# Optimization experiments

Hardware: AMD Instinct MI355X
Metric: run time of the kernel (lower is better)

Reference implementation:

```python
import jax, jax.numpy as jnp
import numpy as np

B, S, D, H, E = 4, 2048, 1024, 4096, 8


def setup_inputs() -> dict:
    key = jax.random.key(0)
    ks = jax.random.split(key, 8)
    w = lambda k, shape: (jax.random.normal(k, shape, jnp.float32) * 0.02)
    return {
        "x": jax.random.normal(ks[0], (B, S, D), jnp.float32),
        "noise_eps": jax.random.normal(ks[1], (B, S, E), jnp.float32),
        "Wg": w(ks[2], (D, E)), "bg": jnp.zeros((E,), jnp.float32),
        "Wn": w(ks[3], (D, E)), "bn": jnp.zeros((E,), jnp.float32),
        "W1": w(ks[4], (E, D, H)), "b1": jnp.zeros((E, H), jnp.float32),
        "W2": w(ks[5], (E, H, D)), "b2": jnp.zeros((E, D), jnp.float32),
        "top_k": 2,
    }


def reference(x, noise_eps, Wg, bg, Wn, bn, W1, b1, W2, b2, top_k):
    b, s, d = x.shape
    e = Wg.shape[1]
    xt = x.reshape(-1, d)            # [T, D] flattened tokens
    eps = noise_eps.reshape(-1, e)   # [T, E]

    # Noisy top-k router
    logits = xt @ Wg + bg                                   # [T, E]
    noisy = logits + eps * jax.nn.softplus(xt @ Wn + bn)    # [T, E]
    top_vals, top_idx = jax.lax.top_k(noisy, top_k)         # [T, k]

    # sparse logits: -inf everywhere except top-k, then softmax -> 0 gate off-topk
    rows = jnp.arange(xt.shape[0])[:, None]
    sparse = jnp.full_like(noisy, -jnp.inf).at[rows, top_idx].set(top_vals)
    gate = jax.nn.softmax(sparse, axis=-1)                  # [T, E], zeros off-topk

    # Expert MLPs (exact GELU, as nn.GELU default); gate==0 off-topk reproduces
    # the masked gather/scatter combine of the original exactly.
    out = jnp.zeros_like(xt)
    for i in range(e):  # small fixed expert count
        h = jax.nn.gelu(xt @ W1[i] + b1[i], approximate=False)  # [T, H]
        o = h @ W2[i] + b2[i]                                   # [T, D]
        out = out + o * gate[:, i:i + 1]
    return out.reshape(b, s, d)
```

## Files before the change

kernel.cpp:

```cpp
#include <hip/hip_runtime.h>
#include <hip/hip_bf16.h>
#include <cmath>

#define T_TOK 8192
#define E_NUM 8
#define D_DIM 1024
#define H_DIM 4096

typedef __attribute__((ext_vector_type(4))) short bf16x4;
typedef __attribute__((ext_vector_type(8))) short bf16x8;
typedef __attribute__((ext_vector_type(4))) float f32x4;

__device__ __forceinline__ unsigned short f2bf(float f) {
  union { float f; unsigned u; } v; v.f = f;
  unsigned r = v.u + 0x7fffu + ((v.u >> 16) & 1u);
  return (unsigned short)(r >> 16);
}

__device__ __forceinline__ void gload_lds16(const void* g, void* l) {
  __builtin_amdgcn_global_load_lds(
      (const __attribute__((address_space(1))) unsigned int*)g,
      (__attribute__((address_space(3))) unsigned int*)l, 16, 0, 0);
}


__global__ void __launch_bounds__(256) cvt_x_kernel(const float* __restrict__ x,
                                                    ushort* __restrict__ xb) {
  int i = blockIdx.x * 256 + threadIdx.x;
  float4 v = ((const float4*)x)[i];
  ushort4 o;
  o.x = f2bf(v.x); o.y = f2bf(v.y); o.z = f2bf(v.z); o.w = f2bf(v.w);
  int u = i & 7;
  int oi = (i & ~7) | (((u & 3) << 1) | (u >> 2));
  ((ushort4*)xb)[oi] = o;
}

__global__ void __launch_bounds__(256) transpose_cvt_kernel(
    const float* __restrict__ src, ushort* __restrict__ dst, int K, int N) {
  __shared__ __align__(16) float tile[64][68];
  size_t eoff = (size_t)blockIdx.z * K * N;
  int n0 = blockIdx.x * 64, k0 = blockIdx.y * 64;
  int t = threadIdx.x;
  int kr = t >> 4, nc = (t & 15) * 4;
#pragma unroll
  for (int i = 0; i < 4; ++i) {
    float4 v = *(const float4*)(src + eoff + (size_t)(k0 + kr + i * 16) * N + n0 + nc);
    *(float4*)&tile[kr + i * 16][nc] = v;
  }
  __syncthreads();
  int n = t >> 3, s = t & 7, g = s >> 2, p = s & 3;
#pragma unroll
  for (int j = 0; j < 2; ++j) {
    int nn = n + j * 32;
    union { bf16x8 v8; ushort e[8]; } o;
#pragma unroll
    for (int h = 0; h < 2; ++h)
#pragma unroll
      for (int r = 0; r < 4; ++r) {
        int k = g * 32 + h * 16 + p * 4 + r;
        o.e[h * 4 + r] = f2bf(tile[k][nn]);
      }
    *(bf16x8*)(dst + eoff + (size_t)(n0 + nn) * K + k0 + g * 32 + p * 8) = o.v8;
  }
}

__global__ void __launch_bounds__(256) router_kernel(
    const float* __restrict__ x, const float* __restrict__ eps,
    const float* __restrict__ Wg, const float* __restrict__ bg,
    const float* __restrict__ Wn, const float* __restrict__ bn,
    int* __restrict__ tok, float* __restrict__ gateL, int* __restrict__ cnt) {
  int lane = threadIdx.x & 63;
  int t = blockIdx.x * 4 + (threadIdx.x >> 6);
  float ag[8], an[8];
#pragma unroll
  for (int e = 0; e < 8; ++e) { ag[e] = 0.f; an[e] = 0.f; }
  const float* xr = x + (size_t)t * D_DIM;
#pragma unroll 4
  for (int i = 0; i < 16; ++i) {
    int d = lane + i * 64;
    float xv = xr[d];
    const float4* g4 = (const float4*)(Wg + d * 8);
    const float4* n4 = (const float4*)(Wn + d * 8);
    float4 ga = g4[0], gb = g4[1], na = n4[0], nb = n4[1];
    ag[0] += xv * ga.x; ag[1] += xv * ga.y; ag[2] += xv * ga.z; ag[3] += xv * ga.w;
    ag[4] += xv * gb.x; ag[5] += xv * gb.y; ag[6] += xv * gb.z; ag[7] += xv * gb.w;
    an[0] += xv * na.x; an[1] += xv * na.y; an[2] += xv * na.z; an[3] += xv * na.w;
    an[4] += xv * nb.x; an[5] += xv * nb.y; an[6] += xv * nb.z; an[7] += xv * nb.w;
  }
#pragma unroll
  for (int off = 32; off > 0; off >>= 1) {
#pragma unroll
    for (int e = 0; e < 8; ++e) {
      ag[e] += __shfl_xor(ag[e], off);
      an[e] += __shfl_xor(an[e], off);
    }
  }
  if (lane == 0) {
    float noisy[8];
#pragma unroll
    for (int e = 0; e < 8; ++e) {
      float lg = ag[e] + bg[e];
      float ln = an[e] + bn[e];
      float sp = (ln > 20.f) ? ln : log1pf(expf(ln));
      noisy[e] = lg + eps[(size_t)t * 8 + e] * sp;
    }
    int i0 = 0; float v0 = noisy[0];
#pragma unroll
    for (int e = 1; e < 8; ++e) if (noisy[e] > v0) { v0 = noisy[e]; i0 = e; }
    int i1 = -1; float v1 = -1e30f;
#pragma unroll
    for (int e = 0; e < 8; ++e) if (e != i0 && noisy[e] > v1) { v1 = noisy[e]; i1 = e; }
    float ee = expf(v1 - v0);
    float g0 = 1.f / (1.f + ee);
    float g1 = ee / (1.f + ee);
    int p0 = atomicAdd(cnt + i0, 1);
    int p1 = atomicAdd(cnt + i1, 1);
    tok[i0 * T_TOK + p0] = t * 2;     gateL[i0 * T_TOK + p0] = g0;
    tok[i1 * T_TOK + p1] = t * 2 + 1; gateL[i1 * T_TOK + p1] = g1;
  }
}

template <int KD, int NC, bool FIRST>
__global__ void __launch_bounds__(256, 2) moe_gemm_kernel(
    const ushort* __restrict__ Abase, const ushort* __restrict__ Bt,
    const float* __restrict__ bias, const int* __restrict__ tok,
    const float* __restrict__ gateL, const int* __restrict__ cnt,
    ushort* __restrict__ hbuf, float* __restrict__ out) {
  constexpr int MT = T_TOK / 128;
  constexpr int NT = NC / 128;
  constexpr int NKT = KD / 64;
  int nwg = MT * NT * E_NUM;
  int q8 = nwg >> 3;
  int bid = blockIdx.x;
  int wg = (bid & 7) * q8 + (bid >> 3);
  int m_t = wg % MT;
  int n_t = (wg / MT) % NT;
  int e = wg / (MT * NT);

  int c = cnt[e];
  int m0 = m_t * 128;
  if (m0 >= c) return;
  int n0 = n_t * 128;

  __shared__ __align__(16) ushort As[2][128 * 64];
  __shared__ __align__(16) ushort Bs[2][128 * 64];
  int tid = threadIdx.x;
  int lane = tid & 63, wave = tid >> 6;
  int wr = (wave >> 1) * 64, wc = (wave & 1) * 64;
  const int* tokE = tok + e * T_TOK;
  const ushort* Be = Bt + (size_t)e * NC * KD;

  int srow = tid >> 3, scol = tid & 7;
  const ushort* asrc[4]; const ushort* bsrc[4];
#pragma unroll
  for (int p = 0; p < 4; ++p) {
    int r = p * 32 + srow;
    int pi = m0 + r;
    int ar = 0;
    if (pi < c) { int tsv = tokE[pi]; ar = FIRST ? (tsv >> 1) : tsv; }
    int sl = (scol ^ (r & 7)) * 8;
    asrc[p] = Abase + (size_t)ar * KD + sl;
    bsrc[p] = Be + (size_t)(n0 + r) * KD + sl;
  }

  f32x4 acc[4][4];
#pragma unroll
  for (int i = 0; i < 4; ++i)
#pragma unroll
    for (int j = 0; j < 4; ++j) {
      f32x4 z = {0.f, 0.f, 0.f, 0.f};
      acc[i][j] = z;
    }

  int r16 = lane & 15;
  int q = lane >> 4;
  int rr = lane & 7;
  int s0 = (q ^ rr) << 4;

#pragma unroll
  for (int p = 0; p < 4; ++p) {
    gload_lds16(asrc[p], (char*)As[0] + p * 4096 + tid * 16);
    gload_lds16(bsrc[p], (char*)Bs[0] + p * 4096 + tid * 16);
  }
  __syncthreads();

  int cur = 0;
  for (int kt = 0; kt < NKT; ++kt) {
    if (kt + 1 < NKT) {
#pragma unroll
      for (int p = 0; p < 4; ++p) {
        gload_lds16(asrc[p] + (kt + 1) * 64, (char*)As[cur ^ 1] + p * 4096 + tid * 16);
        gload_lds16(bsrc[p] + (kt + 1) * 64, (char*)Bs[cur ^ 1] + p * 4096 + tid * 16);
      }
    }
    const char* Ab = (const char*)As[cur];
    const char* Bb = (const char*)Bs[cur];
#pragma unroll
    for (int ks = 0; ks < 2; ++ks) {
      const int so = s0 ^ (ks << 6);
      bf16x8 af[4], bfr[4];
#pragma unroll
      for (int i = 0; i < 4; ++i) {
        af[i]  = *(const bf16x8*)(Ab + (wr + i * 16 + r16) * 128 + so);
        bfr[i] = *(const bf16x8*)(Bb + (wc + i * 16 + r16) * 128 + so);
      }
#pragma unroll
      for (int mi = 0; mi < 4; ++mi)
#pragma unroll
        for (int ni = 0; ni < 4; ++ni)
          acc[mi][ni] = __builtin_amdgcn_mfma_f32_16x16x32_bf16(
              af[mi], bfr[ni], acc[mi][ni], 0, 0, 0);
    }
    __syncthreads();
    cur ^= 1;
  }

  const float* be = bias + (size_t)e * NC;
#pragma unroll
  for (int mi = 0; mi < 4; ++mi) {
#pragma unroll
    for (int r = 0; r < 4; ++r) {
      int rowl = wr + mi * 16 + q * 4 + r;
      int p = m0 + rowl;
      if (p < c) {
        int tsv = tokE[p];
        if (FIRST) {
          ushort* hrow = hbuf + (size_t)tsv * H_DIM;
#pragma unroll
          for (int ni = 0; ni < 4; ++ni) {
            int col = n0 + wc + ni * 16 + r16;
            float v = acc[mi][ni][r] + be[col];
            v = 0.5f * v * (1.f + erff(v * 0.70710678118654752f));
            int pos = ((r16 >> 2) & 3) * 8 + (ni & 1) * 4 + (r16 & 3);
            hrow[(col & ~31) + pos] = f2bf(v);
          }
        } else {
          float g = gateL[e * T_TOK + p];
          float* orow = out + (size_t)(tsv >> 1) * D_DIM;
#pragma unroll
          for (int ni = 0; ni < 4; ++ni) {
            int col = n0 + wc + ni * 16 + r16;
            float v = acc[mi][ni][r] + be[col];
            atomicAdd(&orow[col], g * v);
          }
        }
      }
    }
  }
}

extern "C" void kernel_launch(void* const* d_in, const int* in_sizes, int n_in,
                              void* d_out, int out_size, void* d_ws, size_t ws_size,
                              hipStream_t stream) {
  const float* x   = (const float*)d_in[0];
  const float* eps = (const float*)d_in[1];
  const float* Wg  = (const float*)d_in[2];
  const float* bg  = (const float*)d_in[3];
  const float* Wn  = (const float*)d_in[4];
  const float* bn  = (const float*)d_in[5];
  const float* W1  = (const float*)d_in[6];
  const float* b1  = (const float*)d_in[7];
  const float* W2  = (const float*)d_in[8];
  const float* b2  = (const float*)d_in[9];
  float* out = (float*)d_out;

  const size_t nXB = (size_t)T_TOK * D_DIM;
  const size_t nW1 = (size_t)E_NUM * D_DIM * H_DIM;
  const size_t nHB = (size_t)T_TOK * 2 * H_DIM;
  ushort* xb   = (ushort*)d_ws;
  ushort* W1T  = xb + nXB;
  ushort* W2T  = W1T + nW1;
  ushort* hbuf = W2T + nW1;
  int*   tok   = (int*)(hbuf + nHB);
  float* gateL = (float*)(tok + E_NUM * T_TOK);
  int*   cnt   = (int*)(gateL + E_NUM * T_TOK);
  size_t need = (size_t)((char*)(cnt + 8) - (char*)d_ws);
  if (ws_size < need) return;

  hipMemsetAsync(cnt, 0, 8 * sizeof(int), stream);
  hipMemsetAsync(out, 0, (size_t)out_size * sizeof(float), stream);

  cvt_x_kernel<<<(int)(nXB / 4 / 256), 256, 0, stream>>>(x, xb);
  transpose_cvt_kernel<<<dim3(H_DIM / 64, D_DIM / 64, E_NUM), 256, 0, stream>>>(
      W1, W1T, D_DIM, H_DIM);
  transpose_cvt_kernel<<<dim3(D_DIM / 64, H_DIM / 64, E_NUM), 256, 0, stream>>>(
      W2, W2T, H_DIM, D_DIM);
  router_kernel<<<T_TOK / 4, 256, 0, stream>>>(x, eps, Wg, bg, Wn, bn, tok, gateL, cnt);
  moe_gemm_kernel<D_DIM, H_DIM, true>
      <<<(T_TOK / 128) * (H_DIM / 128) * E_NUM, 256, 0, stream>>>(
          xb, W1T, b1, tok, gateL, cnt, hbuf, out);
  moe_gemm_kernel<H_DIM, D_DIM, false>
      <<<(T_TOK / 128) * (D_DIM / 128) * E_NUM, 256, 0, stream>>>(
          hbuf, W2T, b2, tok, gateL, cnt, hbuf, out);
}
```

Measured before the change: 1.395 ms.

## Compact routed tokens into per-expert padded groups and enlarge GEMM tiles

```diff
diff --git a/kernel.cpp b/kernel.cpp
--- a/kernel.cpp
+++ b/kernel.cpp
@@ -6,6 +6,7 @@
 #define E_NUM 8
 #define D_DIM 1024
 #define H_DIM 4096
+#define GROWS 18432
 
 typedef __attribute__((ext_vector_type(4))) short bf16x4;
 typedef __attribute__((ext_vector_type(8))) short bf16x8;
@@ -23,17 +24,6 @@
       (__attribute__((address_space(3))) unsigned int*)l, 16, 0, 0);
 }
 
-
-__global__ void __launch_bounds__(256) cvt_x_kernel(const float* __restrict__ x,
-                                                    ushort* __restrict__ xb) {
-  int i = blockIdx.x * 256 + threadIdx.x;
-  float4 v = ((const float4*)x)[i];
-  ushort4 o;
-  o.x = f2bf(v.x); o.y = f2bf(v.y); o.z = f2bf(v.z); o.w = f2bf(v.w);
-  int u = i & 7;
-  int oi = (i & ~7) | (((u & 3) << 1) | (u >> 2));
-  ((ushort4*)xb)[oi] = o;
-}
 
 __global__ void __launch_bounds__(256) transpose_cvt_kernel(
     const float* __restrict__ src, ushort* __restrict__ dst, int K, int N) {
@@ -120,54 +110,100 @@
   }
 }
 
-template <int KD, int NC, bool FIRST>
-__global__ void __launch_bounds__(256, 2) moe_gemm_kernel(
+__global__ void plan_kernel(const int* __restrict__ cnt, int* __restrict__ goff) {
+  if (threadIdx.x == 0) {
+    int a = 0; goff[0] = 0;
+#pragma unroll
+    for (int e = 0; e < 8; ++e) { a += (cnt[e] + 255) & ~255; goff[e + 1] = a; }
+  }
+}
+
+__global__ void __launch_bounds__(256) compact_kernel(
+    const float* __restrict__ x, const int* __restrict__ tok,
+    const float* __restrict__ gateL, const int* __restrict__ cnt,
+    const int* __restrict__ goff, ushort* __restrict__ xg,
+    float* __restrict__ gateg, int* __restrict__ rowg) {
+  int idx = blockIdx.x * 256 + threadIdx.x;
+  int g = idx >> 7, ch = idx & 127;
+  int e = 0;
+  while (g >= goff[e + 1]) ++e;
+  int p = g - goff[e];
+  ushort* dst = xg + (size_t)g * D_DIM + ch * 8;
+  if (p < cnt[e]) {
+    int tsv = tok[e * T_TOK + p];
+    int trow = tsv >> 1;
+    int gb = ch >> 2, s = ch & 3;
+    const float* src = x + (size_t)trow * D_DIM + gb * 32;
+    float4 lo = *(const float4*)(src + s * 4);
+    float4 hi = *(const float4*)(src + 16 + s * 4);
+    union { bf16x8 v; ushort u[8]; } o;
+    o.u[0] = f2bf(lo.x); o.u[1] = f2bf(lo.y); o.u[2] = f2bf(lo.z); o.u[3] = f2bf(lo.w);
+    o.u[4] = f2bf(hi.x); o.u[5] = f2bf(hi.y); o.u[6] = f2bf(hi.z); o.u[7] = f2bf(hi.w);
+    *(bf16x8*)dst = o.v;
+    if (ch == 0) { gateg[g] = gateL[e * T_TOK + p]; rowg[g] = trow; }
+  } else {
+    bf16x8 z = {0, 0, 0, 0, 0, 0, 0, 0};
+    *(bf16x8*)dst = z;
+  }
+}
+
+template <int KD, int NC, int BN, bool FIRST>
+__global__ void __launch_bounds__(512, 2) moe_gemm_kernel(
     const ushort* __restrict__ Abase, const ushort* __restrict__ Bt,
-    const float* __restrict__ bias, const int* __restrict__ tok,
-    const float* __restrict__ gateL, const int* __restrict__ cnt,
-    ushort* __restrict__ hbuf, float* __restrict__ out) {
-  constexpr int MT = T_TOK / 128;
-  constexpr int NT = NC / 128;
+    const float* __restrict__ bias, const int* __restrict__ goff,
+    const int* __restrict__ cnt, const float* __restrict__ gateg,
+    const int* __restrict__ rowg, ushort* __restrict__ hbuf,
+    float* __restrict__ out) {
+  constexpr int NMT = GROWS / 256;
+  constexpr int NT = NC / BN;
   constexpr int NKT = KD / 64;
-  int nwg = MT * NT * E_NUM;
+  constexpr int NFRAG = BN / 64;
+  constexpr int WN = BN / 4;
+  constexpr int APL = 4;
+  constexpr int BPL = BN * 8 / 512;
+
+  int nwg = NMT * NT;
   int q8 = nwg >> 3;
   int bid = blockIdx.x;
   int wg = (bid & 7) * q8 + (bid >> 3);
-  int m_t = wg % MT;
-  int n_t = (wg / MT) % NT;
-  int e = wg / (MT * NT);
-
-  int c = cnt[e];
-  int m0 = m_t * 128;
-  if (m0 >= c) return;
-  int n0 = n_t * 128;
-
-  __shared__ __align__(16) ushort As[2][128 * 64];
-  __shared__ __align__(16) ushort Bs[2][128 * 64];
+  int mt = wg % NMT;
+  int n_t = wg / NMT;
+
+  int m0g = mt * 256;
+  if (m0g >= goff[8]) return;
+  int e = 0;
+  while (m0g >= goff[e + 1]) ++e;
+  int glim = goff[e] + cnt[e];
+  int n0 = n_t * BN;
+
+  __shared__ __align__(16) ushort As[2][256 * 64];
+  __shared__ __align__(16) ushort Bs[2][BN * 64];
+
   int tid = threadIdx.x;
   int lane = tid & 63, wave = tid >> 6;
-  int wr = (wave >> 1) * 64, wc = (wave & 1) * 64;
-  const int* tokE = tok + e * T_TOK;
+  int wm = wave >> 2, wn = wave & 3;
+
+  const ushort* asrc[APL];
+#pragma unroll
+  for (int p = 0; p < APL; ++p) {
+    int sidx = p * 512 + tid;
+    int row = sidx >> 3, sc = sidx & 7;
+    asrc[p] = Abase + (size_t)(m0g + row) * KD + (sc ^ (row & 7)) * 8;
+  }
+  const ushort* bsrc[BPL];
   const ushort* Be = Bt + (size_t)e * NC * KD;
-
-  int srow = tid >> 3, scol = tid & 7;
-  const ushort* asrc[4]; const ushort* bsrc[4];
-#pragma unroll
-  for (int p = 0; p < 4; ++p) {
-    int r = p * 32 + srow;
-    int pi = m0 + r;
-    int ar = 0;
-    if (pi < c) { int tsv = tokE[pi]; ar = FIRST ? (tsv >> 1) : tsv; }
-    int sl = (scol ^ (r & 7)) * 8;
-    asrc[p] = Abase + (size_t)ar * KD + sl;
-    bsrc[p] = Be + (size_t)(n0 + r) * KD + sl;
-  }
-
-  f32x4 acc[4][4];
-#pragma unroll
-  for (int i = 0; i < 4; ++i)
-#pragma unroll
-    for (int j = 0; j < 4; ++j) {
+#pragma unroll
+  for (int p = 0; p < BPL; ++p) {
+    int sidx = p * 512 + tid;
+    int row = sidx >> 3, sc = sidx & 7;
+    bsrc[p] = Be + (size_t)(n0 + row) * KD + (sc ^ (row & 7)) * 8;
+  }
+
+  f32x4 acc[8][NFRAG];
+#pragma unroll
+  for (int i = 0; i < 8; ++i)
+#pragma unroll
+    for (int j = 0; j < NFRAG; ++j) {
       f32x4 z = {0.f, 0.f, 0.f, 0.f};
       acc[i][j] = z;
     }
@@ -178,38 +214,41 @@
   int s0 = (q ^ rr) << 4;
 
 #pragma unroll
-  for (int p = 0; p < 4; ++p) {
-    gload_lds16(asrc[p], (char*)As[0] + p * 4096 + tid * 16);
-    gload_lds16(bsrc[p], (char*)Bs[0] + p * 4096 + tid * 16);
-  }
+  for (int p = 0; p < APL; ++p)
+    gload_lds16(asrc[p], (char*)As[0] + (p * 512 + tid) * 16);
+#pragma unroll
+  for (int p = 0; p < BPL; ++p)
+    gload_lds16(bsrc[p], (char*)Bs[0] + (p * 512 + tid) * 16);
   __syncthreads();
 
   int cur = 0;
   for (int kt = 0; kt < NKT; ++kt) {
     if (kt + 1 < NKT) {
 #pragma unroll
-      for (int p = 0; p < 4; ++p) {
-        gload_lds16(asrc[p] + (kt + 1) * 64, (char*)As[cur ^ 1] + p * 4096 + tid * 16);
-        gload_lds16(bsrc[p] + (kt + 1) * 64, (char*)Bs[cur ^ 1] + p * 4096 + tid * 16);
-      }
+      for (int p = 0; p < APL; ++p)
+        gload_lds16(asrc[p] + (kt + 1) * 64, (char*)As[cur ^ 1] + (p * 512 + tid) * 16);
+#pragma unroll
+      for (int p = 0; p < BPL; ++p)
+        gload_lds16(bsrc[p] + (kt + 1) * 64, (char*)Bs[cur ^ 1] + (p * 512 + tid) * 16);
     }
     const char* Ab = (const char*)As[cur];
     const char* Bb = (const char*)Bs[cur];
 #pragma unroll
     for (int ks = 0; ks < 2; ++ks) {
       const int so = s0 ^ (ks << 6);
-      bf16x8 af[4], bfr[4];
-#pragma unroll
-      for (int i = 0; i < 4; ++i) {
-        af[i]  = *(const bf16x8*)(Ab + (wr + i * 16 + r16) * 128 + so);
-        bfr[i] = *(const bf16x8*)(Bb + (wc + i * 16 + r16) * 128 + so);
-      }
-#pragma unroll
-      for (int mi = 0; mi < 4; ++mi)
-#pragma unroll
-        for (int ni = 0; ni < 4; ++ni)
-          acc[mi][ni] = __builtin_amdgcn_mfma_f32_16x16x32_bf16(
-              af[mi], bfr[ni], acc[mi][ni], 0, 0, 0);
+      bf16x8 af[8], bf[NFRAG];
+#pragma unroll
+      for (int i = 0; i < 8; ++i)
+        af[i] = *(const bf16x8*)(Ab + (wm * 128 + i * 16 + r16) * 128 + so);
+#pragma unroll
+      for (int j = 0; j < NFRAG; ++j)
+        bf[j] = *(const bf16x8*)(Bb + (wn * WN + j * 16 + r16) * 128 + so);
+#pragma unroll
+      for (int mi = 0; mi < 8; ++mi)
+#pragma unroll
+        for (int nj = 0; nj < NFRAG; ++nj)
+          acc[mi][nj] = __builtin_amdgcn_mfma_f32_16x16x32_bf16(
+              af[mi], bf[nj], acc[mi][nj], 0, 0, 0);
     }
     __syncthreads();
     cur ^= 1;
@@ -217,31 +256,29 @@
 
   const float* be = bias + (size_t)e * NC;
 #pragma unroll
-  for (int mi = 0; mi < 4; ++mi) {
+  for (int mi = 0; mi < 8; ++mi) {
 #pragma unroll
     for (int r = 0; r < 4; ++r) {
-      int rowl = wr + mi * 16 + q * 4 + r;
-      int p = m0 + rowl;
-      if (p < c) {
-        int tsv = tokE[p];
+      int grow = m0g + wm * 128 + mi * 16 + q * 4 + r;
+      if (grow < glim) {
         if (FIRST) {
-          ushort* hrow = hbuf + (size_t)tsv * H_DIM;
-#pragma unroll
-          for (int ni = 0; ni < 4; ++ni) {
-            int col = n0 + wc + ni * 16 + r16;
-            float v = acc[mi][ni][r] + be[col];
+          ushort* hrow = hbuf + (size_t)grow * H_DIM;
+#pragma unroll
+          for (int nj = 0; nj < NFRAG; ++nj) {
+            int col = n0 + wn * WN + nj * 16 + r16;
+            float v = acc[mi][nj][r] + be[col];
             v = 0.5f * v * (1.f + erff(v * 0.70710678118654752f));
-            int pos = ((r16 >> 2) & 3) * 8 + (ni & 1) * 4 + (r16 & 3);
+            int pos = ((r16 >> 2) & 3) * 8 + (nj & 1) * 4 + (r16 & 3);
             hrow[(col & ~31) + pos] = f2bf(v);
           }
         } else {
-          float g = gateL[e * T_TOK + p];
-          float* orow = out + (size_t)(tsv >> 1) * D_DIM;
-#pragma unroll
-          for (int ni = 0; ni < 4; ++ni) {
-            int col = n0 + wc + ni * 16 + r16;
-            float v = acc[mi][ni][r] + be[col];
-            atomicAdd(&orow[col], g * v);
+          float gt = gateg[grow];
+          float* orow = out + (size_t)rowg[grow] * D_DIM;
+#pragma unroll
+          for (int nj = 0; nj < NFRAG; ++nj) {
+            int col = n0 + wn * WN + nj * 16 + r16;
+            float v = acc[mi][nj][r] + be[col];
+            atomicAdd(&orow[col], gt * v);
           }
         }
       }
@@ -264,32 +301,35 @@
   const float* b2  = (const float*)d_in[9];
   float* out = (float*)d_out;
 
-  const size_t nXB = (size_t)T_TOK * D_DIM;
-  const size_t nW1 = (size_t)E_NUM * D_DIM * H_DIM;
-  const size_t nHB = (size_t)T_TOK * 2 * H_DIM;
-  ushort* xb   = (ushort*)d_ws;
-  ushort* W1T  = xb + nXB;
-  ushort* W2T  = W1T + nW1;
-  ushort* hbuf = W2T + nW1;
-  int*   tok   = (int*)(hbuf + nHB);
+  const size_t nW = (size_t)E_NUM * D_DIM * H_DIM;
+  ushort* W1T  = (ushort*)d_ws;
+  ushort* W2T  = W1T + nW;
+  ushort* xg   = W2T + nW;
+  ushort* hbuf = xg + (size_t)GROWS * D_DIM;
+  int*   tok   = (int*)(hbuf + (size_t)GROWS * H_DIM);
   float* gateL = (float*)(tok + E_NUM * T_TOK);
   int*   cnt   = (int*)(gateL + E_NUM * T_TOK);
-  size_t need = (size_t)((char*)(cnt + 8) - (char*)d_ws);
+  int*   goff  = cnt + 8;
+  float* gateg = (float*)(goff + 16);
+  int*   rowg  = (int*)(gateg + GROWS);
+  size_t need = (size_t)((char*)(rowg + GROWS) - (char*)d_ws);
   if (ws_size < need) return;
 
   hipMemsetAsync(cnt, 0, 8 * sizeof(int), stream);
   hipMemsetAsync(out, 0, (size_t)out_size * sizeof(float), stream);
 
-  cvt_x_kernel<<<(int)(nXB / 4 / 256), 256, 0, stream>>>(x, xb);
   transpose_cvt_kernel<<<dim3(H_DIM / 64, D_DIM / 64, E_NUM), 256, 0, stream>>>(
       W1, W1T, D_DIM, H_DIM);
   transpose_cvt_kernel<<<dim3(D_DIM / 64, H_DIM / 64, E_NUM), 256, 0, stream>>>(
       W2, W2T, H_DIM, D_DIM);
   router_kernel<<<T_TOK / 4, 256, 0, stream>>>(x, eps, Wg, bg, Wn, bn, tok, gateL, cnt);
-  moe_gemm_kernel<D_DIM, H_DIM, true>
-      <<<(T_TOK / 128) * (H_DIM / 128) * E_NUM, 256, 0, stream>>>(
-          xb, W1T, b1, tok, gateL, cnt, hbuf, out);
-  moe_gemm_kernel<H_DIM, D_DIM, false>
-      <<<(T_TOK / 128) * (D_DIM / 128) * E_NUM, 256, 0, stream>>>(
-          hbuf, W2T, b2, tok, gateL, cnt, hbuf, out);
-}
+  plan_kernel<<<1, 64, 0, stream>>>(cnt, goff);
+  compact_kernel<<<GROWS * 128 / 256, 256, 0, stream>>>(
+      x, tok, gateL, cnt, goff, xg, gateg, rowg);
+  moe_gemm_kernel<D_DIM, H_DIM, 256, true>
+      <<<(GROWS / 256) * (H_DIM / 256), 512, 0, stream>>>(
+          xg, W1T, b1, goff, cnt, gateg, rowg, hbuf, out);
+  moe_gemm_kernel<H_DIM, D_DIM, 128, false>
+      <<<(GROWS / 256) * (D_DIM / 128), 512, 0, stream>>>(
+          hbuf, W2T, b2, goff, cnt, gateg, rowg, hbuf, out);
+}
```

New measurement: 1.259 ms. 9.8% less time.
